# Performance work log

Measured on AMD Instinct MI355X. Metric: run time of the kernel, lower is better.

The kernel has to match this reference:

```python
import jax, jax.numpy as jnp
import numpy as np

D_MODEL = 1024
N_HEADS = 16
B, T = 2, 2048


def setup_inputs() -> dict:
    key = jax.random.key(0)
    kx, kqkv, ko = jax.random.split(key, 3)
    x = jax.random.normal(kx, (B, T, D_MODEL), dtype=jnp.float32)
    # flax Linear default init (lecun_normal ~ scaled); plain scaled normal is fine for a baseline
    Wqkv = jax.random.normal(kqkv, (D_MODEL, 3 * D_MODEL), dtype=jnp.float32) / np.sqrt(D_MODEL)
    Wo = jax.random.normal(ko, (D_MODEL, D_MODEL), dtype=jnp.float32) / np.sqrt(D_MODEL)
    return {"x": x, "Wqkv": Wqkv, "Wo": Wo}


def reference(x, Wqkv, Wo):
    Bx, Tx, C = x.shape
    H = N_HEADS
    Hd = C // H
    scale = C ** (-0.5)  # NOTE: module scales by d_model**-0.5, not head_dim**-0.5
    qkv = x @ Wqkv  # [B, T, 3C]
    q, k, v = jnp.split(qkv, 3, axis=-1)
    q = q.reshape(Bx, Tx, H, Hd).transpose(0, 2, 1, 3)  # [B,H,T,Hd]
    k = k.reshape(Bx, Tx, H, Hd).transpose(0, 2, 1, 3)
    v = v.reshape(Bx, Tx, H, Hd).transpose(0, 2, 1, 3)
    attn = jnp.einsum('bhid,bhjd->bhij', q, k) * scale  # [B,H,T,T]
    mask = jnp.tril(jnp.ones((Tx, Tx), dtype=jnp.bool_))
    attn = jnp.where(mask[None, None], attn, jnp.finfo(attn.dtype).min)
    attn = jax.nn.softmax(attn.astype(jnp.float32), axis=-1).astype(attn.dtype)
    out = jnp.einsum('bhij,bhjd->bhid', attn, v)  # [B,H,T,Hd]
    out = out.transpose(0, 2, 1, 3).reshape(Bx, Tx, C)
    return out @ Wo
```

## Files before the change

### kernel.cpp

```cpp
#include <hip/hip_runtime.h>
#include <cstdint>
#include <math.h>

#define D_MODEL 1024
#define N_HEADS 16
#define HEAD_DIM 64
#define BB 2
#define TT 2048
#define QSCALE 0.04508422002778011f
#define MSTATIC 12.0f

typedef float f32x4 __attribute__((ext_vector_type(4)));
typedef __bf16 bf16x8 __attribute__((ext_vector_type(8)));

__device__ inline ushort f2bf(float f) {
    union { float f; uint32_t u; } c; c.f = f;
    uint32_t u = c.u;
    uint32_t r = (u + 0x7FFFu + ((u >> 16) & 1u)) >> 16;
    return (ushort)r;
}
__device__ inline ushort f2bf_hw(float f) {
    __bf16 h = (__bf16)f;
    return __builtin_bit_cast(ushort, h);
}

__device__ inline void load_lds16(const ushort* g, ushort* lds_uniform_base) {
    __builtin_amdgcn_global_load_lds(
        (const __attribute__((address_space(1))) uint32_t*)g,
        (__attribute__((address_space(3))) uint32_t*)lds_uniform_base, 16, 0, 0);
}

__global__ __launch_bounds__(256) void prep(
    const float4* __restrict__ xin, ushort4* __restrict__ xb,
    const float* __restrict__ Wqkv, ushort* __restrict__ WqkvT,
    const float* __restrict__ Wo, ushort* __restrict__ WoT)
{
    int bid = blockIdx.x;
    int tid = threadIdx.x;
    if (bid < 4096) {
        int i = bid * 256 + tid;
        float4 v = xin[i];
        ushort4 u;
        u.x = f2bf(v.x); u.y = f2bf(v.y); u.z = f2bf(v.z); u.w = f2bf(v.w);
        xb[i] = u;
        return;
    }
    __shared__ ushort tile[32][33];
    int tx = tid & 31, ty = tid >> 5;
    const float* in; ushort* out; int R, C, c0, r0;
    if (bid < 7168) {
        int b2 = bid - 4096;
        in = Wqkv; out = WqkvT; R = D_MODEL; C = 3 * D_MODEL;
        c0 = (b2 % 96) * 32; r0 = (b2 / 96) * 32;
    } else {
        int b3 = bid - 7168;
        in = Wo; out = WoT; R = D_MODEL; C = D_MODEL;
        c0 = (b3 % 32) * 32; r0 = (b3 / 32) * 32;
    }
#pragma unroll
    for (int i = 0; i < 32; i += 8)
        tile[ty + i][tx] = f2bf(in[(size_t)(r0 + ty + i) * C + (c0 + tx)]);
    __syncthreads();
#pragma unroll
    for (int i = 0; i < 32; i += 8)
        out[(size_t)(c0 + ty + i) * R + (r0 + tx)] = tile[tx][ty + i];
}

__global__ __launch_bounds__(256) void transpose_v_bf16(
    const ushort* __restrict__ in, ushort* __restrict__ out)
{
    int z = blockIdx.z;
    const ushort* ip = in + (size_t)z * TT * HEAD_DIM;
    ushort* op = out + (size_t)z * TT * HEAD_DIM;
    __shared__ ushort tile[32][33];
    int tx = threadIdx.x, ty = threadIdx.y;
    int d0 = blockIdx.x * 32;
    int t0 = blockIdx.y * 32;
#pragma unroll
    for (int i = 0; i < 32; i += 8)
        tile[ty + i][tx] = ip[(size_t)(t0 + ty + i) * HEAD_DIM + d0 + tx];
    __syncthreads();
#pragma unroll
    for (int i = 0; i < 32; i += 8)
        op[(size_t)(d0 + ty + i) * TT + t0 + tx] = tile[tx][ty + i];
}

__device__ inline void gemm128_mainloop(
    const ushort* __restrict__ A, const ushort* __restrict__ BT,
    int rowBase, int colBase, ushort* Al, ushort* Bl,
    f32x4 acc[4][4], int wave, int lane)
{
    const int K = D_MODEL;
    int lr = lane & 15, quad = lane >> 4;
    int lrow = lane >> 2;
    int kq = lane & 3;
    int mq = (wave >> 1) * 64, nq = (wave & 1) * 64;

    const ushort* gA0 = A + (size_t)(rowBase + wave * 32 + lrow) * K + kq * 8;
    const ushort* gA1 = gA0 + (size_t)16 * K;
    const ushort* gB0 = BT + (size_t)(colBase + wave * 32 + lrow) * K + kq * 8;
    const ushort* gB1 = gB0 + (size_t)16 * K;
    ushort* lA0 = Al + (wave * 32) * 32;
    ushort* lA1 = Al + (wave * 32 + 16) * 32;
    ushort* lB0 = Bl + (wave * 32) * 32;
    ushort* lB1 = Bl + (wave * 32 + 16) * 32;

    for (int kt = 0; kt < K / 32; ++kt) {
        __syncthreads();
        int ko = kt * 32;
        load_lds16(gA0 + ko, lA0);
        load_lds16(gA1 + ko, lA1);
        load_lds16(gB0 + ko, lB0);
        load_lds16(gB1 + ko, lB1);
        __syncthreads();
        bf16x8 af[4], bf[4];
#pragma unroll
        for (int mi = 0; mi < 4; ++mi)
            af[mi] = *(const bf16x8*)(Al + (mq + mi * 16 + lr) * 32 + quad * 8);
#pragma unroll
        for (int ni = 0; ni < 4; ++ni)
            bf[ni] = *(const bf16x8*)(Bl + (nq + ni * 16 + lr) * 32 + quad * 8);
#pragma unroll
        for (int mi = 0; mi < 4; ++mi)
#pragma unroll
            for (int ni = 0; ni < 4; ++ni)
                acc[mi][ni] = __builtin_amdgcn_mfma_f32_16x16x32_bf16(
                    af[mi], bf[ni], acc[mi][ni], 0, 0, 0);
    }
}

__global__ __launch_bounds__(256) void gemm_qkv(
    const ushort* __restrict__ A, const ushort* __restrict__ BT,
    ushort* __restrict__ Qo, ushort* __restrict__ Ko, ushort* __restrict__ Vo)
{
    __shared__ ushort Al[128 * 32];
    __shared__ ushort Bl[128 * 32];
    int tid = threadIdx.x;
    int wave = tid >> 6, lane = tid & 63;
    int lr = lane & 15, quad = lane >> 4;
    int rowBase = blockIdx.y * 128;
    int colBase = blockIdx.x * 128;
    f32x4 acc[4][4] = {};
    gemm128_mainloop(A, BT, rowBase, colBase, Al, Bl, acc, wave, lane);

    int mq = (wave >> 1) * 64, nq = (wave & 1) * 64;
#pragma unroll
    for (int ni = 0; ni < 4; ++ni) {
        int n = colBase + nq + ni * 16 + lr;
        int s = n >> 10;
        int cc = n & 1023;
        int h = cc >> 6, d = cc & 63;
        ushort* dst = (s == 0) ? Qo : (s == 1 ? Ko : Vo);
        float scale = (s == 0) ? QSCALE : 1.0f;
#pragma unroll
        for (int mi = 0; mi < 4; ++mi) {
#pragma unroll
            for (int i = 0; i < 4; ++i) {
                int m = rowBase + mq + mi * 16 + quad * 4 + i;
                int b = m >> 11, t = m & 2047;
                int bh = b * N_HEADS + h;
                dst[((size_t)bh * TT + t) * HEAD_DIM + d] = f2bf(acc[mi][ni][i] * scale);
            }
        }
    }
}

__global__ __launch_bounds__(256) void gemm_plain(
    const ushort* __restrict__ A, const ushort* __restrict__ BT,
    float* __restrict__ O, int N)
{
    const int K = D_MODEL;
    __shared__ ushort Al[128 * 32];
    __shared__ ushort Bl[64 * 32];
    int tid = threadIdx.x;
    int wave = tid >> 6, lane = tid & 63;
    int lr = lane & 15, quad = lane >> 4;
    int lrow = lane >> 2, kq = lane & 3;
    int rowBase = blockIdx.y * 128;
    int colBase = blockIdx.x * 64;
    int mq = (wave >> 1) * 64, nq = (wave & 1) * 32;

    const ushort* gA0 = A + (size_t)(rowBase + wave * 32 + lrow) * K + kq * 8;
    const ushort* gA1 = gA0 + (size_t)16 * K;
    const ushort* gB0 = BT + (size_t)(colBase + wave * 32 + lrow) * K + kq * 8;
    const ushort* gB1 = gB0 + (size_t)16 * K;
    ushort* lA0 = Al + (wave * 32) * 32;
    ushort* lA1 = Al + (wave * 32 + 16) * 32;
    ushort* lB0 = Bl + (wave * 32) * 32;
    ushort* lB1 = Bl + (wave * 32 + 16) * 32;

    f32x4 acc[4][2] = {};
    for (int kt = 0; kt < K / 32; ++kt) {
        __syncthreads();
        int ko = kt * 32;
        load_lds16(gA0 + ko, lA0);
        load_lds16(gA1 + ko, lA1);
        if (wave < 2) {
            load_lds16(gB0 + ko, lB0);
            load_lds16(gB1 + ko, lB1);
        }
        __syncthreads();
        bf16x8 af[4], bf[2];
#pragma unroll
        for (int mi = 0; mi < 4; ++mi)
            af[mi] = *(const bf16x8*)(Al + (mq + mi * 16 + lr) * 32 + quad * 8);
#pragma unroll
        for (int ni = 0; ni < 2; ++ni)
            bf[ni] = *(const bf16x8*)(Bl + (nq + ni * 16 + lr) * 32 + quad * 8);
#pragma unroll
        for (int mi = 0; mi < 4; ++mi)
#pragma unroll
            for (int ni = 0; ni < 2; ++ni)
                acc[mi][ni] = __builtin_amdgcn_mfma_f32_16x16x32_bf16(
                    af[mi], bf[ni], acc[mi][ni], 0, 0, 0);
    }

#pragma unroll
    for (int mi = 0; mi < 4; ++mi)
#pragma unroll
        for (int ni = 0; ni < 2; ++ni) {
            int n = colBase + nq + ni * 16 + lr;
#pragma unroll
            for (int i = 0; i < 4; ++i) {
                int m = rowBase + mq + mi * 16 + quad * 4 + i;
                O[(size_t)m * N + n] = acc[mi][ni][i];
            }
        }
}

__global__ __launch_bounds__(256) void attn_flash(
    const ushort* __restrict__ Q,
    const ushort* __restrict__ K,
    const ushort* __restrict__ VT,
    ushort* __restrict__ AO)
{
    int bid = blockIdx.x;
    int bh  = bid & 31;
    int idx = bid >> 5;
    int qi  = (idx < 8) ? idx : (23 - idx);
    int tid = threadIdx.x;
    int wave = tid >> 6, lane = tid & 63;
    int quad = lane >> 4, lr = lane & 15;
    int qb = qi * 128;
    int qw = qb + wave * 32;

    const ushort* Qb = Q  + (size_t)bh * TT * HEAD_DIM;
    const ushort* Kb = K  + (size_t)bh * TT * HEAD_DIM;
    const ushort* Vb = VT + (size_t)bh * HEAD_DIM * TT;

    __shared__ ushort Kl[8 * 64 * 8];
    __shared__ ushort Vl[8 * 64 * 8];
    __shared__ ushort pbuf[4][32][40];
    ushort (*P)[40] = pbuf[wave];

    const ushort* gK0 = Kb + (size_t)lane * HEAD_DIM + wave * 8;
    const ushort* gK1 = Kb + (size_t)lane * HEAD_DIM + (wave + 4) * 8;
    const ushort* gV0 = Vb + (size_t)lane * TT + wave * 8;
    const ushort* gV1 = Vb + (size_t)lane * TT + 32 + wave * 8;
    ushort* lK0 = Kl + wave * 512;
    ushort* lK1 = Kl + (wave + 4) * 512;
    ushort* lV0 = Vl + wave * 512;
    ushort* lV1 = Vl + (wave + 4) * 512;

    bf16x8 qa[2][2];
#pragma unroll
    for (int r = 0; r < 2; ++r)
#pragma unroll
        for (int s = 0; s < 2; ++s)
            qa[r][s] = *(const bf16x8*)(Qb + (size_t)(qw + r * 16 + lr) * HEAD_DIM
                                           + s * 32 + quad * 8);

    f32x4 o[2][4] = {};
    f32x4 l[2] = {};

    bf16x8 ones;
#pragma unroll
    for (int j = 0; j < 8; ++j) ones[j] = (__bf16)1.0f;

    int myktiles = (qw >> 5) + 1;
    int tiles64 = (qb >> 6) + 2;

    for (int kt64 = 0; kt64 < tiles64; ++kt64) {
        size_t koff = (size_t)kt64 * 64;
        __syncthreads();
        load_lds16(gK0 + koff * HEAD_DIM, lK0);
        load_lds16(gK1 + koff * HEAD_DIM, lK1);
        load_lds16(gV0 + koff, lV0);
        load_lds16(gV1 + koff, lV1);
        __syncthreads();

#pragma unroll
        for (int sub = 0; sub < 2; ++sub) {
            int kt32 = kt64 * 2 + sub;
            if (kt32 >= myktiles) break;

            bf16x8 kb[2][2];
#pragma unroll
            for (int c = 0; c < 2; ++c)
#pragma unroll
                for (int s = 0; s < 2; ++s)
                    kb[c][s] = *(const bf16x8*)&Kl[(((s * 4 + quad) * 64)
                                 + sub * 32 + c * 16 + lr) * 8];
            bf16x8 vb[4];
#pragma unroll
            for (int d = 0; d < 4; ++d)
                vb[d] = *(const bf16x8*)&Vl[(((sub * 4 + quad) * 64)
                             + d * 16 + lr) * 8];

            f32x4 sc[2][2];
#pragma unroll
            for (int r = 0; r < 2; ++r)
#pragma unroll
                for (int c = 0; c < 2; ++c)
#pragma unroll
                    for (int i = 0; i < 4; ++i) sc[r][c][i] = -MSTATIC;
#pragma unroll
            for (int r = 0; r < 2; ++r)
#pragma unroll
                for (int c = 0; c < 2; ++c) {
                    sc[r][c] = __builtin_amdgcn_mfma_f32_16x16x32_bf16(qa[r][0], kb[c][0], sc[r][c], 0, 0, 0);
                    sc[r][c] = __builtin_amdgcn_mfma_f32_16x16x32_bf16(qa[r][1], kb[c][1], sc[r][c], 0, 0, 0);
                }
            if (kt32 == myktiles - 1) {
#pragma unroll
                for (int r = 0; r < 2; ++r)
#pragma unroll
                    for (int c = 0; c < 2; ++c)
#pragma unroll
                        for (int i = 0; i < 4; ++i)
                            if (c * 16 + lr > r * 16 + quad * 4 + i) sc[r][c][i] = -3e38f;
            }

#pragma unroll
            for (int r = 0; r < 2; ++r)
#pragma unroll
                for (int c = 0; c < 2; ++c)
#pragma unroll
                    for (int i = 0; i < 4; ++i)
                        P[r * 16 + quad * 4 + i][c * 16 + lr] =
                            f2bf_hw(__builtin_amdgcn_exp2f(sc[r][c][i]));

#pragma unroll
            for (int r = 0; r < 2; ++r) {
                bf16x8 pa = *(const bf16x8*)&P[r * 16 + lr][quad * 8];
                l[r] = __builtin_amdgcn_mfma_f32_16x16x32_bf16(pa, ones, l[r], 0, 0, 0);
#pragma unroll
                for (int d = 0; d < 4; ++d)
                    o[r][d] = __builtin_amdgcn_mfma_f32_16x16x32_bf16(pa, vb[d], o[r][d], 0, 0, 0);
            }
        }
    }

    int b = bh >> 4, h = bh & 15;
#pragma unroll
    for (int r = 0; r < 2; ++r) {
        f32x4 rl;
#pragma unroll
        for (int i = 0; i < 4; ++i) rl[i] = 1.0f / l[r][i];
#pragma unroll
        for (int d = 0; d < 4; ++d)
#pragma unroll
            for (int i = 0; i < 4; ++i) {
                int row = qw + r * 16 + quad * 4 + i;
                AO[((size_t)(b * TT + row)) * D_MODEL + h * HEAD_DIM + d * 16 + lr] =
                    f2bf(o[r][d][i] * rl[i]);
            }
    }
}

extern "C" void kernel_launch(void* const* d_in, const int* in_sizes, int n_in,
                              void* d_out, int out_size, void* d_ws, size_t ws_size,
                              hipStream_t stream)
{
    (void)in_sizes; (void)n_in; (void)out_size; (void)ws_size;
    const float* x    = (const float*)d_in[0];
    const float* Wqkv = (const float*)d_in[1];
    const float* Wo   = (const float*)d_in[2];
    float* out = (float*)d_out;

    char* ws = (char*)d_ws;
    size_t off = 0;
    ushort* WqkvT = (ushort*)(ws + off); off += (size_t)3 * D_MODEL * D_MODEL * 2;
    ushort* WoT   = (ushort*)(ws + off); off += (size_t)D_MODEL * D_MODEL * 2;
    ushort* xb    = (ushort*)(ws + off); off += (size_t)BB * TT * D_MODEL * 2;
    ushort* Qd    = (ushort*)(ws + off); off += (size_t)BB * D_MODEL * TT * 2;
    ushort* Kd    = (ushort*)(ws + off); off += (size_t)BB * D_MODEL * TT * 2;
    ushort* Vd    = (ushort*)(ws + off); off += (size_t)BB * D_MODEL * TT * 2;
    ushort* VTd   = (ushort*)(ws + off); off += (size_t)BB * D_MODEL * TT * 2;
    ushort* AO    = (ushort*)(ws + off); off += (size_t)BB * TT * D_MODEL * 2;

    prep<<<dim3(8192), 256, 0, stream>>>(
        (const float4*)x, (ushort4*)xb, Wqkv, WqkvT, Wo, WoT);

    gemm_qkv<<<dim3(3 * D_MODEL / 128, BB * TT / 128), 256, 0, stream>>>(
        xb, WqkvT, Qd, Kd, Vd);

    transpose_v_bf16<<<dim3(HEAD_DIM / 32, TT / 32, BB * N_HEADS), dim3(32, 8), 0, stream>>>(
        Vd, VTd);

    attn_flash<<<dim3(512), 256, 0, stream>>>(Qd, Kd, VTd, AO);

    gemm_plain<<<dim3(D_MODEL / 64, BB * TT / 128), 256, 0, stream>>>(
        AO, WoT, out, D_MODEL);
}
```

Baseline: 204.2 us.

## Double-buffer K/V LDS tiles to overlap global loads with attention compute

The flash-attention loop now keeps two LDS buffers for K and V. The next 64-key tile is prefetched with direct-to-LDS loads while the current tile is consumed, with manual vmcnt waits and raw s_barrier in place of two __syncthreads per iteration. This is meant to hide global-load latency behind the MFMA work. It doubles the K/V LDS footprint, which may reduce occupancy, and relies on hand-counted waitcnt correctness.

New measurement: 206.1 us. Within noise of the previous version (+1.0%).

```diff
diff --git a/kernel.cpp b/kernel.cpp
--- a/kernel.cpp
+++ b/kernel.cpp
@@ -248,8 +248,8 @@
     const ushort* Kb = K  + (size_t)bh * TT * HEAD_DIM;
     const ushort* Vb = VT + (size_t)bh * HEAD_DIM * TT;
 
-    __shared__ ushort Kl[8 * 64 * 8];
-    __shared__ ushort Vl[8 * 64 * 8];
+    __shared__ ushort Kl[2][8 * 64 * 8];
+    __shared__ ushort Vl[2][8 * 64 * 8];
     __shared__ ushort pbuf[4][32][40];
     ushort (*P)[40] = pbuf[wave];
 
@@ -257,10 +257,6 @@
     const ushort* gK1 = Kb + (size_t)lane * HEAD_DIM + (wave + 4) * 8;
     const ushort* gV0 = Vb + (size_t)lane * TT + wave * 8;
     const ushort* gV1 = Vb + (size_t)lane * TT + 32 + wave * 8;
-    ushort* lK0 = Kl + wave * 512;
-    ushort* lK1 = Kl + (wave + 4) * 512;
-    ushort* lV0 = Vl + wave * 512;
-    ushort* lV1 = Vl + (wave + 4) * 512;
 
     bf16x8 qa[2][2];
 #pragma unroll
@@ -280,14 +276,32 @@
     int myktiles = (qw >> 5) + 1;
     int tiles64 = (qb >> 6) + 2;
 
+    load_lds16(gK0, Kl[0] + wave * 512);
+    load_lds16(gK1, Kl[0] + (wave + 4) * 512);
+    load_lds16(gV0, Vl[0] + wave * 512);
+    load_lds16(gV1, Vl[0] + (wave + 4) * 512);
+
     for (int kt64 = 0; kt64 < tiles64; ++kt64) {
-        size_t koff = (size_t)kt64 * 64;
-        __syncthreads();
-        load_lds16(gK0 + koff * HEAD_DIM, lK0);
-        load_lds16(gK1 + koff * HEAD_DIM, lK1);
-        load_lds16(gV0 + koff, lV0);
-        load_lds16(gV1 + koff, lV1);
-        __syncthreads();
+        int cur = kt64 & 1;
+        __builtin_amdgcn_s_barrier();
+        if (kt64 + 1 < tiles64) {
+            size_t koff = (size_t)(kt64 + 1) * 64;
+            ushort* KlN = Kl[cur ^ 1];
+            ushort* VlN = Vl[cur ^ 1];
+            load_lds16(gK0 + koff * HEAD_DIM, KlN + wave * 512);
+            load_lds16(gK1 + koff * HEAD_DIM, KlN + (wave + 4) * 512);
+            load_lds16(gV0 + koff, VlN + wave * 512);
+            load_lds16(gV1 + koff, VlN + (wave + 4) * 512);
+            asm volatile("s_waitcnt vmcnt(4)" ::: "memory");
+        } else {
+            asm volatile("s_waitcnt vmcnt(0)" ::: "memory");
+        }
+        __builtin_amdgcn_sched_barrier(0);
+        __builtin_amdgcn_s_barrier();
+        __builtin_amdgcn_sched_barrier(0);
+
+        const ushort* Klc = Kl[cur];
+        const ushort* Vlc = Vl[cur];
 
 #pragma unroll
         for (int sub = 0; sub < 2; ++sub) {
@@ -299,12 +313,12 @@
             for (int c = 0; c < 2; ++c)
 #pragma unroll
                 for (int s = 0; s < 2; ++s)
-                    kb[c][s] = *(const bf16x8*)&Kl[(((s * 4 + quad) * 64)
+                    kb[c][s] = *(const bf16x8*)&Klc[(((s * 4 + quad) * 64)
                                  + sub * 32 + c * 16 + lr) * 8];
             bf16x8 vb[4];
 #pragma unroll
             for (int d = 0; d < 4; ++d)
-                vb[d] = *(const bf16x8*)&Vl[(((sub * 4 + quad) * 64)
+                vb[d] = *(const bf16x8*)&Vlc[(((sub * 4 + quad) * 64)
                              + d * 16 + lr) * 8];
 
             f32x4 sc[2][2];
```

## Pair low and high 16-row query groups per wave for causal load balance

Applied to the files above, without the earlier changes.

Each wave now handles two 16-row query groups, one from the front and one from the back of the sequence (a and 127-a), so every wave does roughly equal causal work. The block-to-(head, tile) mapping changes to 16 blocks per head, and each block loops over a number of K/V tiles set by its largest row group. The low group skips computation once past its causal limit. This aims to remove wave-level imbalance inside a block and the tail imbalance across blocks. The cost is that the low group sits idle while the high group finishes, which adds branching inside the loop.

After: 199.4 us. 2.4% less time.

```diff
diff --git a/kernel.cpp b/kernel.cpp
--- a/kernel.cpp
+++ b/kernel.cpp
@@ -235,14 +235,20 @@
     ushort* __restrict__ AO)
 {
     int bid = blockIdx.x;
-    int bh  = bid & 31;
-    int idx = bid >> 5;
-    int qi  = (idx < 8) ? idx : (23 - idx);
+    int bh  = bid >> 4;
+    int idx = bid & 15;
     int tid = threadIdx.x;
     int wave = tid >> 6, lane = tid & 63;
     int quad = lane >> 4, lr = lane & 15;
-    int qb = qi * 128;
-    int qw = qb + wave * 32;
+
+    int a    = idx * 4 + wave;
+    int Gl   = a;
+    int Gh   = 127 - a;
+    int rowl = Gl << 4;
+    int rowh = Gh << 4;
+    int liml = Gl >> 1;
+    int limh = Gh >> 1;
+    int bt64 = 32 - idx;
 
     const ushort* Qb = Q  + (size_t)bh * TT * HEAD_DIM;
     const ushort* Kb = K  + (size_t)bh * TT * HEAD_DIM;
@@ -264,11 +270,13 @@
 
     bf16x8 qa[2][2];
 #pragma unroll
-    for (int r = 0; r < 2; ++r)
+    for (int r = 0; r < 2; ++r) {
+        int rb = (r == 0) ? rowl : rowh;
 #pragma unroll
         for (int s = 0; s < 2; ++s)
-            qa[r][s] = *(const bf16x8*)(Qb + (size_t)(qw + r * 16 + lr) * HEAD_DIM
+            qa[r][s] = *(const bf16x8*)(Qb + (size_t)(rb + lr) * HEAD_DIM
                                            + s * 32 + quad * 8);
+    }
 
     f32x4 o[2][4] = {};
     f32x4 l[2] = {};
@@ -277,10 +285,7 @@
 #pragma unroll
     for (int j = 0; j < 8; ++j) ones[j] = (__bf16)1.0f;
 
-    int myktiles = (qw >> 5) + 1;
-    int tiles64 = (qb >> 6) + 2;
-
-    for (int kt64 = 0; kt64 < tiles64; ++kt64) {
+    for (int kt64 = 0; kt64 < bt64; ++kt64) {
         size_t koff = (size_t)kt64 * 64;
         __syncthreads();
         load_lds16(gK0 + koff * HEAD_DIM, lK0);
@@ -292,7 +297,8 @@
 #pragma unroll
         for (int sub = 0; sub < 2; ++sub) {
             int kt32 = kt64 * 2 + sub;
-            if (kt32 >= myktiles) break;
+            if (kt32 > limh) break;
+            int act0 = (kt32 <= liml);
 
             bf16x8 kb[2][2];
 #pragma unroll
@@ -307,41 +313,41 @@
                 vb[d] = *(const bf16x8*)&Vl[(((sub * 4 + quad) * 64)
                              + d * 16 + lr) * 8];
 
-            f32x4 sc[2][2];
-#pragma unroll
-            for (int r = 0; r < 2; ++r)
+#pragma unroll
+            for (int r = 0; r < 2; ++r) {
+                if (r == 0 && !act0) continue;
+                int rb  = (r == 0) ? rowl : rowh;
+                int lim = (r == 0) ? liml : limh;
+
+                f32x4 sc[2];
 #pragma unroll
                 for (int c = 0; c < 2; ++c)
 #pragma unroll
-                    for (int i = 0; i < 4; ++i) sc[r][c][i] = -MSTATIC;
-#pragma unroll
-            for (int r = 0; r < 2; ++r)
+                    for (int i = 0; i < 4; ++i) sc[c][i] = -MSTATIC;
 #pragma unroll
                 for (int c = 0; c < 2; ++c) {
-                    sc[r][c] = __builtin_amdgcn_mfma_f32_16x16x32_bf16(qa[r][0], kb[c][0], sc[r][c], 0, 0, 0);
-                    sc[r][c] = __builtin_amdgcn_mfma_f32_16x16x32_bf16(qa[r][1], kb[c][1], sc[r][c], 0, 0, 0);
+                    sc[c] = __builtin_amdgcn_mfma_f32_16x16x32_bf16(qa[r][0], kb[c][0], sc[c], 0, 0, 0);
+                    sc[c] = __builtin_amdgcn_mfma_f32_16x16x32_bf16(qa[r][1], kb[c][1], sc[c], 0, 0, 0);
                 }
-            if (kt32 == myktiles - 1) {
-#pragma unroll
-                for (int r = 0; r < 2; ++r)
+                if (kt32 == lim) {
 #pragma unroll
                     for (int c = 0; c < 2; ++c)
 #pragma unroll
                         for (int i = 0; i < 4; ++i)
-                            if (c * 16 + lr > r * 16 + quad * 4 + i) sc[r][c][i] = -3e38f;
-            }
-
-#pragma unroll
-            for (int r = 0; r < 2; ++r)
+                            if (kt32 * 32 + c * 16 + lr > rb + quad * 4 + i)
+                                sc[c][i] = -3e38f;
+                }
 #pragma unroll
                 for (int c = 0; c < 2; ++c)
 #pragma unroll
                     for (int i = 0; i < 4; ++i)
                         P[r * 16 + quad * 4 + i][c * 16 + lr] =
-                            f2bf_hw(__builtin_amdgcn_exp2f(sc[r][c][i]));
+                            f2bf_hw(__builtin_amdgcn_exp2f(sc[c][i]));
+            }
 
 #pragma unroll
             for (int r = 0; r < 2; ++r) {
+                if (r == 0 && !act0) continue;
                 bf16x8 pa = *(const bf16x8*)&P[r * 16 + lr][quad * 8];
                 l[r] = __builtin_amdgcn_mfma_f32_16x16x32_bf16(pa, ones, l[r], 0, 0, 0);
 #pragma unroll
@@ -354,6 +360,7 @@
     int b = bh >> 4, h = bh & 15;
 #pragma unroll
     for (int r = 0; r < 2; ++r) {
+        int rb = (r == 0) ? rowl : rowh;
         f32x4 rl;
 #pragma unroll
         for (int i = 0; i < 4; ++i) rl[i] = 1.0f / l[r][i];
@@ -361,7 +368,7 @@
         for (int d = 0; d < 4; ++d)
 #pragma unroll
             for (int i = 0; i < 4; ++i) {
-                int row = qw + r * 16 + quad * 4 + i;
+                int row = rb + quad * 4 + i;
                 AO[((size_t)(b * TT + row)) * D_MODEL + h * HEAD_DIM + d * 16 + lr] =
                     f2bf(o[r][d][i] * rl[i]);
             }
```
